# Optimization experiments

Measured on AMD Instinct MI355X. Metric: run time of the kernel, lower is better.

The kernel has to match this reference:

```python
import jax, jax.numpy as jnp
import numpy as np

B, S, D = 2, 1024, 1024
R = 512          # rank (attn) == knowledge_rank
N = 32           # neurons per pool (6 pools)
DS = 64          # router d_space
TOP_K = 4
N_HEADS = 16
LN_EPS = 1e-6


def _ln(x, scale, bias):
    mu = jnp.mean(x, axis=-1, keepdims=True)
    var = jnp.mean(jnp.square(x - mu), axis=-1, keepdims=True)
    return (x - mu) * jax.lax.rsqrt(var + LN_EPS) * scale + bias


def _topk_sparsify(w, k):
    vals, idx = jax.lax.top_k(w, k)
    oh = jax.nn.one_hot(idx, w.shape[-1], dtype=w.dtype)
    sp = (oh * vals[..., None]).sum(axis=-2)
    return sp / (sp.sum(axis=-1, keepdims=True) + 1e-8)


def _feature(x, neurons, w):
    # x:[B,S,D] neurons:[N,D,R] w:[B,S,N] -> [B,S,R]; dense [B,S,N,R] intermediate (the kernel target)
    all_h = jnp.einsum('bsd,ndr->bsnr', x, neurons)
    return jnp.einsum('bsnr,bsn->bsr', all_h, w)


def _restore(h, neurons, w):
    # h:[B,S,R] neurons:[N,R,D] w:[B,S,N] -> [B,S,D]
    all_o = jnp.einsum('bsr,nrd->bsnd', h, neurons)
    return jnp.einsum('bsnd,bsn->bsd', all_o, w)


def _route(h, emb_seg, k):
    logits = jnp.einsum('bsd,nd->bsn', h, emb_seg)
    return _topk_sparsify(jax.nn.softmax(logits, axis=-1), k)


def setup_inputs():
    key = jax.random.key(0)
    ks = jax.random.split(key, 16)
    sn = lambda k, sh: jax.random.normal(k, sh, jnp.float32) * 0.02
    return {
        'x': jax.random.normal(ks[0], (B, S, D), jnp.float32),
        'f_qk': sn(ks[1], (N, D, R)),
        'f_v': sn(ks[2], (N, D, R)),
        'r_qk': sn(ks[3], (N, R, D)),
        'r_v': sn(ks[4], (N, R, D)),
        'f_know': sn(ks[5], (N, D, R)),
        'r_know': sn(ks[6], (N, R, D)),
        'neuron_emb': sn(ks[7], (6 * N, DS)),
        'W_all': sn(ks[8], (D, 6 * DS)),
        'b_all': jnp.zeros((6 * DS,), jnp.float32),
        'W_fk': sn(ks[9], (D, DS)),
        'b_fk': jnp.zeros((DS,), jnp.float32),
        'W_rk': sn(ks[10], (D, DS)),
        'b_rk': jnp.zeros((DS,), jnp.float32),
        'W_o': sn(ks[11], (D, D)),
        'ln1_s': jnp.ones((D,), jnp.float32),
        'ln1_b': jnp.zeros((D,), jnp.float32),
        'ln2_s': jnp.ones((D,), jnp.float32),
        'ln2_b': jnp.zeros((D,), jnp.float32),
        'top_k': TOP_K,
        'n_heads': N_HEADS,
    }


def reference(x, f_qk, f_v, r_qk, r_v, f_know, r_know, neuron_emb,
              W_all, b_all, W_fk, b_fk, W_rk, b_rk, W_o,
              ln1_s, ln1_b, ln2_s, ln2_b, top_k, n_heads):
    Bx, Sx, Dm = x.shape
    n = f_qk.shape[0]
    emb = neuron_emb / (jnp.linalg.norm(neuron_emb, axis=-1, keepdims=True) + 1e-8)
    e_fqk, e_fv, e_rqk, e_rv, e_fk, e_rk = [emb[i * n:(i + 1) * n] for i in range(6)]

    # --- attention circuit (pre-norm) ---
    nx = _ln(x, ln1_s, ln1_b)
    h_all = nx @ W_all + b_all                    # [B,S,6*DS]
    h_fq, h_fk_, h_fv, h_rq, h_rk_, h_rv = jnp.split(h_all, 6, axis=-1)
    w_fq = _route(h_fq, e_fqk, top_k)             # Q/K share the qk neuron pools
    w_fk = _route(h_fk_, e_fqk, top_k)
    w_fv = _route(h_fv, e_fv, top_k)
    w_rq = _route(h_rq, e_rqk, top_k)
    w_rk = _route(h_rk_, e_rqk, top_k)
    w_rv = _route(h_rv, e_rv, top_k)

    Q = _restore(_feature(nx, f_qk, w_fq), r_qk, w_rq)
    K = _restore(_feature(nx, f_qk, w_fk), r_qk, w_rk)
    V = _restore(_feature(nx, f_v, w_fv), r_v, w_rv)

    d_head = Dm // n_heads
    Q = Q.reshape(Bx, Sx, n_heads, d_head).transpose(0, 2, 1, 3)
    K = K.reshape(Bx, Sx, n_heads, d_head).transpose(0, 2, 1, 3)
    V = V.reshape(Bx, Sx, n_heads, d_head).transpose(0, 2, 1, 3)
    scores = jnp.einsum('bhsd,bhtd->bhst', Q, K) / jnp.sqrt(jnp.float32(d_head))
    causal = jnp.tril(jnp.ones((Sx, Sx), dtype=jnp.bool_))
    scores = jnp.where(causal, scores, jnp.finfo(scores.dtype).min)
    attn = jax.nn.softmax(scores, axis=-1)
    out = jnp.einsum('bhst,bhtd->bhsd', attn, V).transpose(0, 2, 1, 3).reshape(Bx, Sx, Dm)
    x = x + out @ W_o

    # --- knowledge circuit (pre-norm) ---
    nx2 = _ln(x, ln2_s, ln2_b)
    w_fknow = _route(nx2 @ W_fk + b_fk, e_fk, top_k)
    w_rknow = _route(nx2 @ W_rk + b_rk, e_rk, top_k)
    x = x + _restore(_feature(nx2, f_know, w_fknow), r_know, w_rknow)
    return x
```

## Files before the change

kernel.cpp:

```cpp
#include <hip/hip_runtime.h>
#include <hip/hip_bf16.h>
#include <cstdint>

#define BS     2048
#define DMODEL 1024
#define RANK   512
#define NEXP   32
#define DSP    64
#define NHEAD  16
#define DHEAD  64
#define SEQ    1024
#define BATCH  2
#define HALL_N 384
#define WSTR   ((size_t)BS * NEXP)
#define LSTR   ((size_t)NEXP * BS)

typedef unsigned short u16;
typedef unsigned int u32;
typedef __attribute__((ext_vector_type(8))) short short8;
typedef __attribute__((ext_vector_type(4))) float f32x4;

__device__ __forceinline__ u16 bfbits(float x) {
  __hip_bfloat16 h = __float2bfloat16(x);
  return __builtin_bit_cast(u16, h);
}
__device__ __forceinline__ float b2f(u16 u) {
  unsigned int x = (unsigned int)u << 16;
  return __builtin_bit_cast(float, x);
}

__global__ void ln_kernel(const float* __restrict__ x,
                          const float* __restrict__ sc,
                          const float* __restrict__ bi,
                          float* __restrict__ out,
                          u16* __restrict__ outb) {
  int tok = blockIdx.x;
  int t = threadIdx.x;
  const float4* xr = reinterpret_cast<const float4*>(x + (size_t)tok * DMODEL);
  float4 v = xr[t];
  float s = v.x + v.y + v.z + v.w;
  float q = v.x * v.x + v.y * v.y + v.z * v.z + v.w * v.w;
#pragma unroll
  for (int off = 32; off > 0; off >>= 1) {
    s += __shfl_xor(s, off);
    q += __shfl_xor(q, off);
  }
  __shared__ float red[8];
  int wid = t >> 6;
  if ((t & 63) == 0) { red[wid] = s; red[4 + wid] = q; }
  __syncthreads();
  s = red[0] + red[1] + red[2] + red[3];
  q = red[4] + red[5] + red[6] + red[7];
  float mu = s * (1.f / DMODEL);
  float var = q * (1.f / DMODEL) - mu * mu;
  float inv = rsqrtf(var + 1e-6f);
  float4 scv = reinterpret_cast<const float4*>(sc)[t];
  float4 biv = reinterpret_cast<const float4*>(bi)[t];
  float4 r;
  r.x = (v.x - mu) * inv * scv.x + biv.x;
  r.y = (v.y - mu) * inv * scv.y + biv.y;
  r.z = (v.z - mu) * inv * scv.z + biv.z;
  r.w = (v.w - mu) * inv * scv.w + biv.w;
  reinterpret_cast<float4*>(out + (size_t)tok * DMODEL)[t] = r;
  ushort4 ob;
  ob.x = bfbits(r.x); ob.y = bfbits(r.y); ob.z = bfbits(r.z); ob.w = bfbits(r.w);
  reinterpret_cast<ushort4*>(outb + (size_t)tok * DMODEL)[t] = ob;
}

__global__ void embnorm_kernel(const float* __restrict__ e, float* __restrict__ o) {
  int row = blockIdx.x;
  int lane = threadIdx.x;
  float v = e[row * DSP + lane];
  float q = v * v;
#pragma unroll
  for (int off = 32; off > 0; off >>= 1) q += __shfl_xor(q, off);
  o[row * DSP + lane] = v / (sqrtf(q) + 1e-8f);
}

__global__ __launch_bounds__(256) void gemm_splitk(const float* __restrict__ A,
                                                   const float* __restrict__ Bm,
                                                   float* __restrict__ part,
                                                   int M, int N, int K, int kchunk) {
  __shared__ float As[16][65];
  __shared__ float Bs[16][64];
  int n0 = blockIdx.x * 64;
  int m0 = blockIdx.y * 64;
  int kbeg = blockIdx.z * kchunk;
  int t = threadIdx.x;
  int tx = t & 15, ty = t >> 4;
  float c[4][4] = {};
  for (int k0 = kbeg; k0 < kbeg + kchunk; k0 += 16) {
#pragma unroll
    for (int i = 0; i < 4; i++) {
      int idx = t + i * 256;
      int m = idx >> 4, kk = idx & 15;
      As[kk][m] = A[(size_t)(m0 + m) * K + k0 + kk];
    }
#pragma unroll
    for (int i = 0; i < 4; i++) {
      int idx = t + i * 256;
      int kk = idx >> 6, nn = idx & 63;
      Bs[kk][nn] = Bm[(size_t)(k0 + kk) * N + n0 + nn];
    }
    __syncthreads();
#pragma unroll
    for (int kk = 0; kk < 16; kk++) {
      float a[4], b[4];
#pragma unroll
      for (int i = 0; i < 4; i++) a[i] = As[kk][ty + i * 16];
#pragma unroll
      for (int j = 0; j < 4; j++) b[j] = Bs[kk][tx + j * 16];
#pragma unroll
      for (int i = 0; i < 4; i++)
#pragma unroll
        for (int j = 0; j < 4; j++) c[i][j] += a[i] * b[j];
    }
    __syncthreads();
  }
  float* po = part + (size_t)blockIdx.z * M * N;
#pragma unroll
  for (int i = 0; i < 4; i++)
#pragma unroll
    for (int j = 0; j < 4; j++)
      po[(size_t)(m0 + ty + i * 16) * N + n0 + tx + j * 16] = c[i][j];
}

__global__ __launch_bounds__(256) void gemm_splitk2(const float* __restrict__ A,
                                                    const float* __restrict__ B0,
                                                    const float* __restrict__ B1,
                                                    float* __restrict__ part,
                                                    int M, int N, int K, int kchunk) {
  __shared__ float As[16][65];
  __shared__ float Bs[16][64];
  int wsel = blockIdx.z >> 3, ks = blockIdx.z & 7;
  const float* Bm = wsel ? B1 : B0;
  int n0 = blockIdx.x * 64;
  int m0 = blockIdx.y * 64;
  int kbeg = ks * kchunk;
  int t = threadIdx.x;
  int tx = t & 15, ty = t >> 4;
  float c[4][4] = {};
  for (int k0 = kbeg; k0 < kbeg + kchunk; k0 += 16) {
#pragma unroll
    for (int i = 0; i < 4; i++) {
      int idx = t + i * 256;
      int m = idx >> 4, kk = idx & 15;
      As[kk][m] = A[(size_t)(m0 + m) * K + k0 + kk];
    }
#pragma unroll
    for (int i = 0; i < 4; i++) {
      int idx = t + i * 256;
      int kk = idx >> 6, nn = idx & 63;
      Bs[kk][nn] = Bm[(size_t)(k0 + kk) * N + n0 + nn];
    }
    __syncthreads();
#pragma unroll
    for (int kk = 0; kk < 16; kk++) {
      float a[4], b[4];
#pragma unroll
      for (int i = 0; i < 4; i++) a[i] = As[kk][ty + i * 16];
#pragma unroll
      for (int j = 0; j < 4; j++) b[j] = Bs[kk][tx + j * 16];
#pragma unroll
      for (int i = 0; i < 4; i++)
#pragma unroll
        for (int j = 0; j < 4; j++) c[i][j] += a[i] * b[j];
    }
    __syncthreads();
  }
  float* po = part + (size_t)blockIdx.z * M * N;
#pragma unroll
  for (int i = 0; i < 4; i++)
#pragma unroll
    for (int j = 0; j < 4; j++)
      po[(size_t)(m0 + ty + i * 16) * N + n0 + tx + j * 16] = c[i][j];
}

__global__ void reduce_bias_kernel(const float* __restrict__ part,
                                   const float* __restrict__ bias,
                                   float* __restrict__ out,
                                   int MN, int N, int KS) {
  int i = blockIdx.x * 256 + threadIdx.x;
  if (i * 4 >= MN) return;
  float4 s = reinterpret_cast<const float4*>(part)[i];
  for (int ks = 1; ks < KS; ks++) {
    float4 p = reinterpret_cast<const float4*>(part + (size_t)ks * MN)[i];
    s.x += p.x; s.y += p.y; s.z += p.z; s.w += p.w;
  }
  int col = (i * 4) % N;
  float4 b = *reinterpret_cast<const float4*>(bias + col);
  s.x += b.x; s.y += b.y; s.z += b.z; s.w += b.w;
  reinterpret_cast<float4*>(out)[i] = s;
}

__global__ void reduce_bias2_kernel(const float* __restrict__ part,
                                    const float* __restrict__ bias0,
                                    const float* __restrict__ bias1,
                                    float* __restrict__ out,
                                    int MN, int N, int KS) {
  int wsel = blockIdx.y;
  const float* p0 = part + (size_t)wsel * KS * MN;
  const float* bias = wsel ? bias1 : bias0;
  float* o = out + (size_t)wsel * MN;
  int i = blockIdx.x * 256 + threadIdx.x;
  if (i * 4 >= MN) return;
  float4 s = reinterpret_cast<const float4*>(p0)[i];
  for (int ks = 1; ks < KS; ks++) {
    float4 p = reinterpret_cast<const float4*>(p0 + (size_t)ks * MN)[i];
    s.x += p.x; s.y += p.y; s.z += p.z; s.w += p.w;
  }
  int col = (i * 4) % N;
  float4 b = *reinterpret_cast<const float4*>(bias + col);
  s.x += b.x; s.y += b.y; s.z += b.z; s.w += b.w;
  reinterpret_cast<float4*>(o)[i] = s;
}

__global__ void route_kernel(const float* __restrict__ h, size_t roff, int ldh,
                             const float* __restrict__ embn, int R0,
                             float* __restrict__ w8) {
  int tok = blockIdx.x;
  int r = blockIdx.y;
  int gr = R0 + r;
  int pool = (gr < 2) ? 0 : (gr < 3) ? 1 : (gr < 5) ? 2 : (gr < 6) ? 3 : (gr < 7) ? 4 : 5;
  const float* e = embn + (size_t)pool * NEXP * DSP;
  const float* hr = h + (size_t)r * roff;
  float* wout = w8 + (size_t)gr * WSTR;
  int lane = threadIdx.x;
  __shared__ float hs[DSP];
  __shared__ float es[NEXP * DSP];
  hs[lane] = hr[(size_t)tok * ldh + lane];
#pragma unroll
  for (int i = 0; i < NEXP * DSP / 64; i++) es[lane + i * 64] = e[lane + i * 64];
  __syncthreads();
  float logit = -1e30f;
  if (lane < NEXP) {
    float s = 0.f;
#pragma unroll
    for (int d = 0; d < DSP; d++) s += hs[d] * es[lane * DSP + d];
    logit = s;
  }
  float mx = logit;
#pragma unroll
  for (int off = 16; off > 0; off >>= 1) mx = fmaxf(mx, __shfl_xor(mx, off));
  float p = (lane < NEXP) ? __expf(logit - mx) : 0.f;
  float sum = p;
#pragma unroll
  for (int off = 16; off > 0; off >>= 1) sum += __shfl_xor(sum, off);
  p = p / sum;
  float val = p;
  float chosen = 0.f;
  float selsum = 0.f;
#pragma unroll
  for (int it = 0; it < 4; it++) {
    float v = val;
    int vi = lane;
#pragma unroll
    for (int off = 16; off > 0; off >>= 1) {
      float ov = __shfl_xor(v, off);
      int oi = __shfl_xor(vi, off);
      if (ov > v || (ov == v && oi < vi)) { v = ov; vi = oi; }
    }
    if (lane == vi) { chosen = p; val = -1.f; }
    selsum += v;
  }
  if (lane < NEXP) wout[(size_t)tok * NEXP + lane] = chosen / (selsum + 1e-8f);
}

__global__ void bucket_kernel(const float* __restrict__ w8,
                              int* __restrict__ lists,
                              int* __restrict__ slotmap,
                              int* __restrict__ counts, int R0) {
  int n = blockIdx.x;
  int gr = R0 + blockIdx.y;
  const float* w = w8 + (size_t)gr * WSTR;
  int* list = lists + (size_t)gr * LSTR;
  int* smap = slotmap + (size_t)gr * LSTR;
  int lane = threadIdx.x;
  int base = 0;
  for (int t0 = 0; t0 < BS; t0 += 64) {
    int tok = t0 + lane;
    bool act = (w[(size_t)tok * NEXP + n] != 0.f);
    unsigned long long mask = __ballot(act);
    int pos = __popcll(mask & ((1ull << lane) - 1ull));
    if (act) {
      list[n * BS + base + pos] = tok;
      smap[n * BS + tok] = base + pos;
    }
    base += __popcll(mask);
  }
  if (lane == 0) counts[gr * NEXP + n] = base;
}

__global__ void scan32_kernel(const int* __restrict__ counts, int* __restrict__ offs) {
  int r = blockIdx.x;
  int lane = threadIdx.x;
  int c = (lane < NEXP) ? counts[r * NEXP + lane] : 0;
  int s = c;
#pragma unroll
  for (int d = 1; d < NEXP; d <<= 1) {
    int o = __shfl_up(s, d);
    if (lane >= d) s += o;
  }
  if (lane < NEXP) offs[r * NEXP + lane] = s - c;
}

#define TCOL(r, c) ((c) ^ (((((r) >> 2)) & 15) << 1))
__global__ void wconv3_kernel(const float* __restrict__ F0,
                              const float* __restrict__ F1,
                              const float* __restrict__ F2,
                              u16* __restrict__ FT, int K, int NOUT) {
  int z = blockIdx.z;
  int p = z >> 5, e = z & 31;
  const float* Fe = ((p == 0) ? F0 : (p == 1) ? F1 : F2) + (size_t)e * K * NOUT;
  u16* FTe = FT + (size_t)z * K * NOUT;
  int n0 = blockIdx.x * 64, k0 = blockIdx.y * 64;
  __shared__ u16 tile[64][66];
  int t = threadIdx.x;
  int kr = t >> 4, nc = (t & 15) * 4;
#pragma unroll
  for (int pp = 0; pp < 4; pp++) {
    int kk = kr + pp * 16;
    float4 v = *reinterpret_cast<const float4*>(Fe + (size_t)(k0 + kk) * NOUT + n0 + nc);
    tile[nc + 0][TCOL(nc + 0, kk)] = bfbits(v.x);
    tile[nc + 1][TCOL(nc + 1, kk)] = bfbits(v.y);
    tile[nc + 2][TCOL(nc + 2, kk)] = bfbits(v.z);
    tile[nc + 3][TCOL(nc + 3, kk)] = bfbits(v.w);
  }
  __syncthreads();
  int nr = t >> 2, c0 = (t & 3) * 16;
  int key = (nr >> 2) & 15;
  const u32* rowp = reinterpret_cast<const u32*>(&tile[nr][0]);
  u32 u[8];
#pragma unroll
  for (int s = 0; s < 8; s++) u[s] = rowp[((c0 >> 1) + s) ^ key];
  u16* dst = FTe + (size_t)(n0 + nr) * K + k0 + c0;
  *reinterpret_cast<uint4*>(dst) = *reinterpret_cast<uint4*>(&u[0]);
  *reinterpret_cast<uint4*>(dst + 8) = *reinterpret_cast<uint4*>(&u[4]);
}

__global__ __launch_bounds__(256) void expert_gemm_mfma(
    const u16* __restrict__ Xb,
    const u16* __restrict__ FT,
    const int* __restrict__ lists,
    const int* __restrict__ counts,
    const int* __restrict__ offsb,
    u16* __restrict__ Cout,
    int R0, int s0, int s1, int s2,
    size_t xstride, int K, int NOUT) {
  int v = blockIdx.y;
  int r = v >> 5, e = v & 31;
  int gr = R0 + r;
  int cnt = counts[gr * NEXP + e];
  int m0 = blockIdx.z * 128;
  if (m0 >= cnt) return;
  int slot = (r == 0) ? s0 : (r == 1) ? s1 : s2;
  int n0 = blockIdx.x * 64;
  const int* list = lists + (size_t)gr * LSTR + (size_t)e * BS;
  __shared__ u16 Xs[128][72];
  __shared__ u16 Fs[64][72];
  __shared__ int toks[128];
  int t = threadIdx.x;
  if (t < 128) toks[t] = (m0 + t < cnt) ? list[m0 + t] : -1;
  __syncthreads();
  const u16* X = Xb + (size_t)r * xstride;
  const u16* FTe = FT + ((size_t)(slot * NEXP + e) * NOUT + n0) * K;
  int wave = t >> 6, lane = t & 63;
  int wm = wave >> 1, wn = wave & 1;
  int lr = lane & 15, kg = lane >> 4;
  f32x4 acc[4][2] = {};
  int xri = t >> 1, xc = (t & 1) * 32;
  int tokr = toks[xri];
  const u16* xrow = X + (size_t)(tokr < 0 ? 0 : tokr) * K + xc;
  int fri = t >> 2, fc = (t & 3) * 16;
  const u16* frow = FTe + (size_t)fri * K + fc;
  short8 xv0 = {}, xv1 = {}, xv2 = {}, xv3 = {}, fv0, fv1;
  if (tokr >= 0) {
    xv0 = *reinterpret_cast<const short8*>(xrow);
    xv1 = *reinterpret_cast<const short8*>(xrow + 8);
    xv2 = *reinterpret_cast<const short8*>(xrow + 16);
    xv3 = *reinterpret_cast<const short8*>(xrow + 24);
  }
  fv0 = *reinterpret_cast<const short8*>(frow);
  fv1 = *reinterpret_cast<const short8*>(frow + 8);
  for (int k0 = 0; k0 < K; k0 += 64) {
    __syncthreads();
    *reinterpret_cast<short8*>(&Xs[xri][xc]) = xv0;
    *reinterpret_cast<short8*>(&Xs[xri][xc + 8]) = xv1;
    *reinterpret_cast<short8*>(&Xs[xri][xc + 16]) = xv2;
    *reinterpret_cast<short8*>(&Xs[xri][xc + 24]) = xv3;
    *reinterpret_cast<short8*>(&Fs[fri][fc]) = fv0;
    *reinterpret_cast<short8*>(&Fs[fri][fc + 8]) = fv1;
    __syncthreads();
    int kn = k0 + 64;
    if (kn < K) {
      if (tokr >= 0) {
        xv0 = *reinterpret_cast<const short8*>(xrow + kn);
        xv1 = *reinterpret_cast<const short8*>(xrow + kn + 8);
        xv2 = *reinterpret_cast<const short8*>(xrow + kn + 16);
        xv3 = *reinterpret_cast<const short8*>(xrow + kn + 24);
      }
      fv0 = *reinterpret_cast<const short8*>(frow + kn);
      fv1 = *reinterpret_cast<const short8*>(frow + kn + 8);
    }
#pragma unroll
    for (int kk = 0; kk < 2; kk++) {
      short8 b0 = *reinterpret_cast<const short8*>(&Fs[wn * 32 + lr][kk * 32 + kg * 8]);
      short8 b1 = *reinterpret_cast<const short8*>(&Fs[wn * 32 + 16 + lr][kk * 32 + kg * 8]);
#pragma unroll
      for (int mi = 0; mi < 4; mi++) {
        short8 a = *reinterpret_cast<const short8*>(&Xs[wm * 64 + mi * 16 + lr][kk * 32 + kg * 8]);
        acc[mi][0] = __builtin_amdgcn_mfma_f32_16x16x32_bf16(a, b0, acc[mi][0], 0, 0, 0);
        acc[mi][1] = __builtin_amdgcn_mfma_f32_16x16x32_bf16(a, b1, acc[mi][1], 0, 0, 0);
      }
    }
  }
  int gbase = r * 4 * BS + offsb[gr * NEXP + e] + m0;
#pragma unroll
  for (int mi = 0; mi < 4; mi++) {
#pragma unroll
    for (int j = 0; j < 4; j++) {
      int row = wm * 64 + mi * 16 + kg * 4 + j;
      if (toks[row] < 0) continue;
      u16* crow = Cout + (size_t)(gbase + row) * NOUT + n0 + wn * 32;
#pragma unroll
      for (int ni = 0; ni < 2; ni++)
        crow[ni * 16 + lr] = bfbits(acc[mi][ni][j]);
    }
  }
}

template <int NOUT, bool FINAL>
__global__ __launch_bounds__(256) void gather_combine(
    const u16* __restrict__ C,
    const float* __restrict__ w8base,
    const int* __restrict__ slotbase,
    const int* __restrict__ offsbase,
    const float* __restrict__ resid,
    float* __restrict__ outf,
    u16* __restrict__ outbase) {
  int tok = blockIdx.x;
  int r = blockIdx.y;
  const float* wr = w8base + (size_t)r * WSTR;
  const int* smap = slotbase + (size_t)r * LSTR;
  const int* offs = offsbase + r * NEXP;
  const u16* Cr = C + (size_t)r * 4 * BS * NOUT;
  int t = threadIdx.x;
  __shared__ float lw[4];
  __shared__ int ls[4];
  __shared__ int lcnt;
  if (t < 64) {
    float wv = (t < NEXP) ? wr[(size_t)tok * NEXP + t] : 0.f;
    bool act = wv != 0.f;
    unsigned long long mask = __ballot(act);
    int pos = __popcll(mask & ((1ull << t) - 1ull));
    if (act) { ls[pos] = offs[t] + smap[t * BS + tok]; lw[pos] = wv; }
    if (t == 0) lcnt = __popcll(mask);
  }
  __syncthreads();
  if (t < NOUT / 4) {
    float4 s = {0.f, 0.f, 0.f, 0.f};
    int cnt = lcnt;
    for (int k = 0; k < cnt; k++) {
      ushort4 v = reinterpret_cast<const ushort4*>(Cr + (size_t)ls[k] * NOUT)[t];
      float wk = lw[k];
      s.x += wk * b2f(v.x); s.y += wk * b2f(v.y);
      s.z += wk * b2f(v.z); s.w += wk * b2f(v.w);
    }
    if (FINAL) {
      float4 rr = reinterpret_cast<const float4*>(resid + (size_t)tok * NOUT)[t];
      s.x += rr.x; s.y += rr.y; s.z += rr.z; s.w += rr.w;
      reinterpret_cast<float4*>(outf + (size_t)tok * NOUT)[t] = s;
    } else {
      ushort4 o;
      o.x = bfbits(s.x); o.y = bfbits(s.y); o.z = bfbits(s.z); o.w = bfbits(s.w);
      reinterpret_cast<ushort4*>(outbase + (size_t)r * BS * NOUT + (size_t)tok * NOUT)[t] = o;
    }
  }
}

template <bool RES>
__global__ __launch_bounds__(256) void dense_gemm_mfma(
    const u16* __restrict__ Ab,
    const u16* __restrict__ BT,
    const float* __restrict__ res,
    float* __restrict__ C, int M, int N, int K) {
  int n0 = blockIdx.x * 64, m0 = blockIdx.y * 64;
  __shared__ u16 Xs[64][72];
  __shared__ u16 Fs[64][72];
  int t = threadIdx.x;
  int wave = t >> 6, lane = t & 63;
  int wm = wave >> 1, wn = wave & 1;
  int lr = lane & 15, kg = lane >> 4;
  f32x4 acc[2][2] = {};
  int srow = t >> 2, sc = (t & 3) * 16;
  const u16* xrow = Ab + (size_t)(m0 + srow) * K + sc;
  const u16* frow = BT + (size_t)(n0 + srow) * K + sc;
  for (int k0 = 0; k0 < K; k0 += 64) {
    short8 xv0 = *reinterpret_cast<const short8*>(xrow + k0);
    short8 xv1 = *reinterpret_cast<const short8*>(xrow + k0 + 8);
    short8 fv0 = *reinterpret_cast<const short8*>(frow + k0);
    short8 fv1 = *reinterpret_cast<const short8*>(frow + k0 + 8);
    __syncthreads();
    *reinterpret_cast<short8*>(&Xs[srow][sc]) = xv0;
    *reinterpret_cast<short8*>(&Xs[srow][sc + 8]) = xv1;
    *reinterpret_cast<short8*>(&Fs[srow][sc]) = fv0;
    *reinterpret_cast<short8*>(&Fs[srow][sc + 8]) = fv1;
    __syncthreads();
#pragma unroll
    for (int kk = 0; kk < 2; kk++) {
      short8 a0 = *reinterpret_cast<const short8*>(&Xs[wm * 32 + lr][kk * 32 + kg * 8]);
      short8 a1 = *reinterpret_cast<const short8*>(&Xs[wm * 32 + 16 + lr][kk * 32 + kg * 8]);
      short8 b0 = *reinterpret_cast<const short8*>(&Fs[wn * 32 + lr][kk * 32 + kg * 8]);
      short8 b1 = *reinterpret_cast<const short8*>(&Fs[wn * 32 + 16 + lr][kk * 32 + kg * 8]);
      acc[0][0] = __builtin_amdgcn_mfma_f32_16x16x32_bf16(a0, b0, acc[0][0], 0, 0, 0);
      acc[0][1] = __builtin_amdgcn_mfma_f32_16x16x32_bf16(a0, b1, acc[0][1], 0, 0, 0);
      acc[1][0] = __builtin_amdgcn_mfma_f32_16x16x32_bf16(a1, b0, acc[1][0], 0, 0, 0);
      acc[1][1] = __builtin_amdgcn_mfma_f32_16x16x32_bf16(a1, b1, acc[1][1], 0, 0, 0);
    }
  }
#pragma unroll
  for (int mi = 0; mi < 2; mi++) {
#pragma unroll
    for (int j = 0; j < 4; j++) {
      int row = m0 + wm * 32 + mi * 16 + kg * 4 + j;
#pragma unroll
      for (int ni = 0; ni < 2; ni++) {
        int col = n0 + wn * 32 + ni * 16 + lr;
        float v = acc[mi][ni][j];
        if (RES) v += res[(size_t)row * N + col];
        C[(size_t)row * N + col] = v;
      }
    }
  }
}

__global__ __launch_bounds__(256) void attn_mfma(const u16* __restrict__ Qb,
                                                 const u16* __restrict__ Kb,
                                                 const u16* __restrict__ Vb,
                                                 u16* __restrict__ Ob) {
  int qt = (gridDim.x - 1 - blockIdx.x) * 64;
  int h = blockIdx.y, b = blockIdx.z;
  int t = threadIdx.x;
  int w = t >> 6, lane = t & 63;
  int lr = lane & 15, kg = lane >> 4;
  __shared__ u16 Ks[64][72];
  __shared__ u16 Vs[64][66];
  __shared__ u16 Ps[4][16][72];
  size_t base = (size_t)(b * SEQ) * DMODEL + (size_t)h * DHEAD;
  const u16* qrow = Qb + base + (size_t)(qt + w * 16 + lr) * DMODEL + kg * 8;
  short8 aq0 = *reinterpret_cast<const short8*>(qrow);
  short8 aq1 = *reinterpret_cast<const short8*>(qrow + 32);
  float m[4], l[4];
#pragma unroll
  for (int j = 0; j < 4; j++) { m[j] = -1e30f; l[j] = 0.f; }
  f32x4 acc_o[4] = {};
  for (int kt = 0; kt <= qt; kt += 64) {
    __syncthreads();
    {
      int r = t >> 2, c0 = (t & 3) * 16;
      const u16* krow = Kb + base + (size_t)(kt + r) * DMODEL + c0;
      *reinterpret_cast<short8*>(&Ks[r][c0]) = *reinterpret_cast<const short8*>(krow);
      *reinterpret_cast<short8*>(&Ks[r][c0 + 8]) = *reinterpret_cast<const short8*>(krow + 8);
      int d = lane;
      int r0v = w * 16;
      const u16* vcol = Vb + base + (size_t)(kt + r0v) * DMODEL + d;
#pragma unroll
      for (int i = 0; i < 16; i++)
        Vs[d][r0v + i] = vcol[(size_t)i * DMODEL];
    }
    __syncthreads();
    f32x4 s[4] = {};
#pragma unroll
    for (int c = 0; c < 4; c++) {
      short8 bk0 = *reinterpret_cast<const short8*>(&Ks[c * 16 + lr][kg * 8]);
      short8 bk1 = *reinterpret_cast<const short8*>(&Ks[c * 16 + lr][32 + kg * 8]);
      s[c] = __builtin_amdgcn_mfma_f32_16x16x32_bf16(aq0, bk0, s[c], 0, 0, 0);
      s[c] = __builtin_amdgcn_mfma_f32_16x16x32_bf16(aq1, bk1, s[c], 0, 0, 0);
    }
#pragma unroll
    for (int c = 0; c < 4; c++)
#pragma unroll
      for (int j = 0; j < 4; j++) s[c][j] *= 0.125f;
    if (kt == qt) {
#pragma unroll
      for (int c = 0; c < 4; c++)
#pragma unroll
        for (int j = 0; j < 4; j++)
          if (c * 16 + lr > w * 16 + kg * 4 + j) s[c][j] = -1e30f;
    }
    float mt[4];
#pragma unroll
    for (int j = 0; j < 4; j++)
      mt[j] = fmaxf(fmaxf(s[0][j], s[1][j]), fmaxf(s[2][j], s[3][j]));
#pragma unroll
    for (int off = 1; off < 16; off <<= 1)
#pragma unroll
      for (int j = 0; j < 4; j++) mt[j] = fmaxf(mt[j], __shfl_xor(mt[j], off));
    float corr[4];
#pragma unroll
    for (int j = 0; j < 4; j++) {
      float mn = fmaxf(m[j], mt[j]);
      corr[j] = __expf(m[j] - mn);
      m[j] = mn;
      l[j] *= corr[j];
    }
#pragma unroll
    for (int di = 0; di < 4; di++)
#pragma unroll
      for (int j = 0; j < 4; j++) acc_o[di][j] *= corr[j];
    float ps[4] = {0.f, 0.f, 0.f, 0.f};
#pragma unroll
    for (int c = 0; c < 4; c++)
#pragma unroll
      for (int j = 0; j < 4; j++) {
        float p = __expf(s[c][j] - m[j]);
        ps[j] += p;
        s[c][j] = p;
      }
#pragma unroll
    for (int off = 1; off < 16; off <<= 1)
#pragma unroll
      for (int j = 0; j < 4; j++) ps[j] += __shfl_xor(ps[j], off);
#pragma unroll
    for (int j = 0; j < 4; j++) l[j] += ps[j];
#pragma unroll
    for (int c = 0; c < 4; c++)
#pragma unroll
      for (int j = 0; j < 4; j++)
        Ps[w][kg * 4 + j][c * 16 + lr] = bfbits(s[c][j]);
    short8 pa0 = *reinterpret_cast<const short8*>(&Ps[w][lr][kg * 8]);
    short8 pa1 = *reinterpret_cast<const short8*>(&Ps[w][lr][32 + kg * 8]);
#pragma unroll
    for (int di = 0; di < 4; di++) {
      short8 bv0 = *reinterpret_cast<const short8*>(&Vs[di * 16 + lr][kg * 8]);
      short8 bv1 = *reinterpret_cast<const short8*>(&Vs[di * 16 + lr][32 + kg * 8]);
      acc_o[di] = __builtin_amdgcn_mfma_f32_16x16x32_bf16(pa0, bv0, acc_o[di], 0, 0, 0);
      acc_o[di] = __builtin_amdgcn_mfma_f32_16x16x32_bf16(pa1, bv1, acc_o[di], 0, 0, 0);
    }
  }
#pragma unroll
  for (int j = 0; j < 4; j++) {
    float inv = 1.f / l[j];
    size_t rowoff = base + (size_t)(qt + w * 16 + kg * 4 + j) * DMODEL;
#pragma unroll
    for (int di = 0; di < 4; di++)
      Ob[rowoff + di * 16 + lr] = bfbits(acc_o[di][j] * inv);
  }
}

extern "C" void kernel_launch(void* const* d_in, const int* in_sizes, int n_in,
                              void* d_out, int out_size, void* d_ws, size_t ws_size,
                              hipStream_t stream) {
  const float* x    = (const float*)d_in[0];
  const float* f_qk = (const float*)d_in[1];
  const float* f_v  = (const float*)d_in[2];
  const float* r_qk = (const float*)d_in[3];
  const float* r_v  = (const float*)d_in[4];
  const float* f_kn = (const float*)d_in[5];
  const float* r_kn = (const float*)d_in[6];
  const float* nemb = (const float*)d_in[7];
  const float* W_all = (const float*)d_in[8];
  const float* b_all = (const float*)d_in[9];
  const float* W_fk  = (const float*)d_in[10];
  const float* b_fk  = (const float*)d_in[11];
  const float* W_rk  = (const float*)d_in[12];
  const float* b_rk  = (const float*)d_in[13];
  const float* W_o   = (const float*)d_in[14];
  const float* ln1s  = (const float*)d_in[15];
  const float* ln1b  = (const float*)d_in[16];
  const float* ln2s  = (const float*)d_in[17];
  const float* ln2b  = (const float*)d_in[18];

  float* ws = (float*)d_ws;
  size_t off = 0;
  auto alloc = [&](size_t nf) { float* p = ws + off; off += nf; return p; };
  float* nx      = alloc((size_t)BS * DMODEL);
  float* nx2     = alloc((size_t)BS * DMODEL);
  float* embn    = alloc(6 * NEXP * DSP);
  float* h_all   = alloc((size_t)BS * HALL_N);
  float* hk2     = alloc((size_t)2 * BS * DSP);
  float* w8      = alloc((size_t)8 * BS * NEXP);
  float* x1      = alloc((size_t)BS * DMODEL);
  float* compactFf = alloc((size_t)3 * 2 * BS * RANK);
  float* compactRf = alloc((size_t)3 * 2 * BS * DMODEL);
  int* lists   = (int*)(ws + off); off += (size_t)8 * NEXP * BS;
  int* slotmap = (int*)(ws + off); off += (size_t)8 * NEXP * BS;
  int* counts  = (int*)(ws + off); off += 8 * NEXP;
  int* offsb   = (int*)(ws + off); off += 8 * NEXP;
  u16* nxb  = (u16*)(ws + off); off += (size_t)BS * DMODEL / 2;
  u16* fqb  = (u16*)(ws + off); off += (size_t)3 * BS * RANK / 2;
  u16* fnb  = (u16*)(ws + off); off += (size_t)BS * RANK / 2;
  u16* Qbb  = (u16*)(ws + off); off += (size_t)3 * BS * DMODEL / 2;
  u16* attnOb = (u16*)(ws + off); off += (size_t)BS * DMODEL / 2;
  u16* woT  = (u16*)(ws + off); off += (size_t)DMODEL * DMODEL / 2;
  u16* wbufF = (u16*)(ws + off); off += (size_t)3 * NEXP * DMODEL * RANK / 2;
  u16* wbufR = (u16*)(ws + off); off += (size_t)3 * NEXP * RANK * DMODEL / 2;
  u16* compactF = (u16*)compactFf;
  u16* compactR = (u16*)compactRf;
  u16* fkb = fqb + (size_t)BS * RANK;
  u16* fvb = fkb + (size_t)BS * RANK;
  u16* Kbb = Qbb + (size_t)BS * DMODEL;
  u16* Vbb = Kbb + (size_t)BS * DMODEL;
  float* h_fk2 = hk2;
  float* partA = compactRf;
  float* partK = compactRf;

  embnorm_kernel<<<6 * NEXP, DSP, 0, stream>>>(nemb, embn);
  wconv3_kernel<<<dim3(RANK / 64, DMODEL / 64, 3 * NEXP), 256, 0, stream>>>(
      f_qk, f_v, f_kn, wbufF, DMODEL, RANK);
  wconv3_kernel<<<dim3(DMODEL / 64, RANK / 64, 3 * NEXP), 256, 0, stream>>>(
      r_qk, r_v, r_kn, wbufR, RANK, DMODEL);
  wconv3_kernel<<<dim3(DMODEL / 64, DMODEL / 64, 1), 256, 0, stream>>>(
      W_o, nullptr, nullptr, woT, DMODEL, DMODEL);

  ln_kernel<<<BS, 256, 0, stream>>>(x, ln1s, ln1b, nx, nxb);
  gemm_splitk<<<dim3(HALL_N / 64, BS / 64, 4), 256, 0, stream>>>(
      nx, W_all, partA, BS, HALL_N, DMODEL, DMODEL / 4);
  reduce_bias_kernel<<<(BS * HALL_N / 4 + 255) / 256, 256, 0, stream>>>(
      partA, b_all, h_all, BS * HALL_N, HALL_N, 4);

  route_kernel<<<dim3(BS, 6), 64, 0, stream>>>(h_all, DSP, HALL_N, embn, 0, w8);
  bucket_kernel<<<dim3(NEXP, 6), 64, 0, stream>>>(w8, lists, slotmap, counts, 0);
  scan32_kernel<<<6, 64, 0, stream>>>(counts, offsb);

  expert_gemm_mfma<<<dim3(RANK / 64, 3 * NEXP, BS / 128), 256, 0, stream>>>(
      nxb, wbufF, lists, counts, offsb, compactF,
      0, 0, 0, 1, 0, DMODEL, RANK);
  gather_combine<RANK, false><<<dim3(BS, 3), 256, 0, stream>>>(
      compactF, w8, slotmap, offsb, nullptr, nullptr, fqb);

  expert_gemm_mfma<<<dim3(DMODEL / 64, 3 * NEXP, BS / 128), 256, 0, stream>>>(
      fqb, wbufR, lists, counts, offsb, compactR,
      3, 0, 0, 1, (size_t)BS * RANK, RANK, DMODEL);
  gather_combine<DMODEL, false><<<dim3(BS, 3), 256, 0, stream>>>(
      compactR, w8 + 3 * WSTR, slotmap + 3 * LSTR, offsb + 3 * NEXP,
      nullptr, nullptr, Qbb);

  attn_mfma<<<dim3(SEQ / 64, NHEAD, BATCH), 256, 0, stream>>>(Qbb, Kbb, Vbb, attnOb);

  dense_gemm_mfma<true><<<dim3(DMODEL / 64, BS / 64), 256, 0, stream>>>(
      attnOb, woT, x, x1, BS, DMODEL, DMODEL);

  ln_kernel<<<BS, 256, 0, stream>>>(x1, ln2s, ln2b, nx2, nxb);
  gemm_splitk2<<<dim3(1, BS / 64, 16), 256, 0, stream>>>(
      nx2, W_fk, W_rk, partK, BS, DSP, DMODEL, DMODEL / 8);
  reduce_bias2_kernel<<<dim3((BS * DSP / 4 + 255) / 256, 2), 256, 0, stream>>>(
      partK, b_fk, b_rk, h_fk2, BS * DSP, DSP, 8);
  route_kernel<<<dim3(BS, 2), 64, 0, stream>>>(h_fk2, (size_t)BS * DSP, DSP, embn, 6, w8);
  bucket_kernel<<<dim3(NEXP, 2), 64, 0, stream>>>(w8, lists, slotmap, counts, 6);
  scan32_kernel<<<2, 64, 0, stream>>>(counts + 6 * NEXP, offsb + 6 * NEXP);

  expert_gemm_mfma<<<dim3(RANK / 64, NEXP, BS / 128), 256, 0, stream>>>(
      nxb, wbufF, lists, counts, offsb, compactF,
      6, 2, 2, 2, 0, DMODEL, RANK);
  gather_combine<RANK, false><<<dim3(BS, 1), 256, 0, stream>>>(
      compactF, w8 + 6 * WSTR, slotmap + 6 * LSTR, offsb + 6 * NEXP,
      nullptr, nullptr, fnb);
  expert_gemm_mfma<<<dim3(DMODEL / 64, NEXP, BS / 128), 256, 0, stream>>>(
      fnb, wbufR, lists, counts, offsb, compactR,
      7, 2, 2, 2, 0, RANK, DMODEL);
  gather_combine<DMODEL, true><<<dim3(BS, 1), 256, 0, stream>>>(
      compactR, w8 + 7 * WSTR, slotmap + 7 * LSTR, offsb + 7 * NEXP,
      x1, (float*)d_out, nullptr);
}
```

Measured before the change: 523.7 us.

## Fuse weight conversions into concurrent routing and expert GEMM launches

Merges the first-stage split-K routing GEMM with the bf16 conversion of the feature weights and W_o into one launch. It also merges the first expert GEMM with the restore-weight conversion, so independent work shares a grid and fills idle CUs. This cuts kernel launches and lets memory-bound conversion overlap compute-bound work. In exchange, shared memory is sized by a union, which may lower occupancy for the conversion blocks, and many expert-GEMM blocks exit early.

```diff
diff --git a/kernel.cpp b/kernel.cpp
--- a/kernel.cpp
+++ b/kernel.cpp
@@ -28,6 +28,12 @@
   unsigned int x = (unsigned int)u << 16;
   return __builtin_bit_cast(float, x);
 }
+
+struct SmemGemm { u16 Xs[128][72]; u16 Fs[64][72]; int toks[128]; };
+struct SmemWc   { u16 tile[64][66]; };
+struct SmemSk   { float As[16][65]; float Bs[16][64]; };
+union SmemSmall { SmemWc w; SmemSk s; };
+union SmemBig   { SmemGemm g; SmemWc w; };
 
 __global__ void ln_kernel(const float* __restrict__ x,
                           const float* __restrict__ sc,
@@ -77,39 +83,36 @@
   o[row * DSP + lane] = v / (sqrtf(q) + 1e-8f);
 }
 
-__global__ __launch_bounds__(256) void gemm_splitk(const float* __restrict__ A,
-                                                   const float* __restrict__ Bm,
-                                                   float* __restrict__ part,
-                                                   int M, int N, int K, int kchunk) {
-  __shared__ float As[16][65];
-  __shared__ float Bs[16][64];
-  int n0 = blockIdx.x * 64;
-  int m0 = blockIdx.y * 64;
-  int kbeg = blockIdx.z * kchunk;
+__device__ __forceinline__ void dev_splitk(const float* __restrict__ A,
+                                           const float* __restrict__ Bm,
+                                           float* __restrict__ part,
+                                           int M, int N, int K, int kchunk,
+                                           int n0, int m0, int ksb, SmemSk* ss) {
   int t = threadIdx.x;
   int tx = t & 15, ty = t >> 4;
+  int kbeg = ksb * kchunk;
   float c[4][4] = {};
   for (int k0 = kbeg; k0 < kbeg + kchunk; k0 += 16) {
 #pragma unroll
     for (int i = 0; i < 4; i++) {
       int idx = t + i * 256;
       int m = idx >> 4, kk = idx & 15;
-      As[kk][m] = A[(size_t)(m0 + m) * K + k0 + kk];
+      ss->As[kk][m] = A[(size_t)(m0 + m) * K + k0 + kk];
     }
 #pragma unroll
     for (int i = 0; i < 4; i++) {
       int idx = t + i * 256;
       int kk = idx >> 6, nn = idx & 63;
-      Bs[kk][nn] = Bm[(size_t)(k0 + kk) * N + n0 + nn];
+      ss->Bs[kk][nn] = Bm[(size_t)(k0 + kk) * N + n0 + nn];
     }
     __syncthreads();
 #pragma unroll
     for (int kk = 0; kk < 16; kk++) {
       float a[4], b[4];
 #pragma unroll
-      for (int i = 0; i < 4; i++) a[i] = As[kk][ty + i * 16];
-#pragma unroll
-      for (int j = 0; j < 4; j++) b[j] = Bs[kk][tx + j * 16];
+      for (int i = 0; i < 4; i++) a[i] = ss->As[kk][ty + i * 16];
+#pragma unroll
+      for (int j = 0; j < 4; j++) b[j] = ss->Bs[kk][tx + j * 16];
 #pragma unroll
       for (int i = 0; i < 4; i++)
 #pragma unroll
@@ -117,7 +120,7 @@
     }
     __syncthreads();
   }
-  float* po = part + (size_t)blockIdx.z * M * N;
+  float* po = part + (size_t)ksb * M * N;
 #pragma unroll
   for (int i = 0; i < 4; i++)
 #pragma unroll
@@ -130,50 +133,10 @@
                                                     const float* __restrict__ B1,
                                                     float* __restrict__ part,
                                                     int M, int N, int K, int kchunk) {
-  __shared__ float As[16][65];
-  __shared__ float Bs[16][64];
+  __shared__ SmemSk ss;
   int wsel = blockIdx.z >> 3, ks = blockIdx.z & 7;
-  const float* Bm = wsel ? B1 : B0;
-  int n0 = blockIdx.x * 64;
-  int m0 = blockIdx.y * 64;
-  int kbeg = ks * kchunk;
-  int t = threadIdx.x;
-  int tx = t & 15, ty = t >> 4;
-  float c[4][4] = {};
-  for (int k0 = kbeg; k0 < kbeg + kchunk; k0 += 16) {
-#pragma unroll
-    for (int i = 0; i < 4; i++) {
-      int idx = t + i * 256;
-      int m = idx >> 4, kk = idx & 15;
-      As[kk][m] = A[(size_t)(m0 + m) * K + k0 + kk];
-    }
-#pragma unroll
-    for (int i = 0; i < 4; i++) {
-      int idx = t + i * 256;
-      int kk = idx >> 6, nn = idx & 63;
-      Bs[kk][nn] = Bm[(size_t)(k0 + kk) * N + n0 + nn];
-    }
-    __syncthreads();
-#pragma unroll
-    for (int kk = 0; kk < 16; kk++) {
-      float a[4], b[4];
-#pragma unroll
-      for (int i = 0; i < 4; i++) a[i] = As[kk][ty + i * 16];
-#pragma unroll
-      for (int j = 0; j < 4; j++) b[j] = Bs[kk][tx + j * 16];
-#pragma unroll
-      for (int i = 0; i < 4; i++)
-#pragma unroll
-        for (int j = 0; j < 4; j++) c[i][j] += a[i] * b[j];
-    }
-    __syncthreads();
-  }
-  float* po = part + (size_t)blockIdx.z * M * N;
-#pragma unroll
-  for (int i = 0; i < 4; i++)
-#pragma unroll
-    for (int j = 0; j < 4; j++)
-      po[(size_t)(m0 + ty + i * 16) * N + n0 + tx + j * 16] = c[i][j];
+  dev_splitk(A, wsel ? B1 : B0, part + (size_t)wsel * 8 * M * N,
+             M, N, K, kchunk, blockIdx.x * 64, blockIdx.y * 64, ks, &ss);
 }
 
 __global__ void reduce_bias_kernel(const float* __restrict__ part,
@@ -305,31 +268,25 @@
 }
 
 #define TCOL(r, c) ((c) ^ (((((r) >> 2)) & 15) << 1))
-__global__ void wconv3_kernel(const float* __restrict__ F0,
-                              const float* __restrict__ F1,
-                              const float* __restrict__ F2,
-                              u16* __restrict__ FT, int K, int NOUT) {
-  int z = blockIdx.z;
-  int p = z >> 5, e = z & 31;
-  const float* Fe = ((p == 0) ? F0 : (p == 1) ? F1 : F2) + (size_t)e * K * NOUT;
-  u16* FTe = FT + (size_t)z * K * NOUT;
-  int n0 = blockIdx.x * 64, k0 = blockIdx.y * 64;
-  __shared__ u16 tile[64][66];
+__device__ __forceinline__ void dev_wconv(const float* __restrict__ Fe,
+                                          u16* __restrict__ FTe,
+                                          int K, int NOUT, int n0, int k0,
+                                          SmemWc* sw) {
   int t = threadIdx.x;
   int kr = t >> 4, nc = (t & 15) * 4;
 #pragma unroll
   for (int pp = 0; pp < 4; pp++) {
     int kk = kr + pp * 16;
     float4 v = *reinterpret_cast<const float4*>(Fe + (size_t)(k0 + kk) * NOUT + n0 + nc);
-    tile[nc + 0][TCOL(nc + 0, kk)] = bfbits(v.x);
-    tile[nc + 1][TCOL(nc + 1, kk)] = bfbits(v.y);
-    tile[nc + 2][TCOL(nc + 2, kk)] = bfbits(v.z);
-    tile[nc + 3][TCOL(nc + 3, kk)] = bfbits(v.w);
+    sw->tile[nc + 0][TCOL(nc + 0, kk)] = bfbits(v.x);
+    sw->tile[nc + 1][TCOL(nc + 1, kk)] = bfbits(v.y);
+    sw->tile[nc + 2][TCOL(nc + 2, kk)] = bfbits(v.z);
+    sw->tile[nc + 3][TCOL(nc + 3, kk)] = bfbits(v.w);
   }
   __syncthreads();
   int nr = t >> 2, c0 = (t & 3) * 16;
   int key = (nr >> 2) & 15;
-  const u32* rowp = reinterpret_cast<const u32*>(&tile[nr][0]);
+  const u32* rowp = reinterpret_cast<const u32*>(&sw->tile[nr][0]);
   u32 u[8];
 #pragma unroll
   for (int s = 0; s < 8; s++) u[s] = rowp[((c0 >> 1) + s) ^ key];
@@ -338,29 +295,20 @@
   *reinterpret_cast<uint4*>(dst + 8) = *reinterpret_cast<uint4*>(&u[4]);
 }
 
-__global__ __launch_bounds__(256) void expert_gemm_mfma(
-    const u16* __restrict__ Xb,
-    const u16* __restrict__ FT,
-    const int* __restrict__ lists,
-    const int* __restrict__ counts,
-    const int* __restrict__ offsb,
-    u16* __restrict__ Cout,
-    int R0, int s0, int s1, int s2,
-    size_t xstride, int K, int NOUT) {
-  int v = blockIdx.y;
+__device__ __forceinline__ void dev_expert_gemm(
+    const u16* __restrict__ Xb, const u16* __restrict__ FT,
+    const int* __restrict__ lists, const int* __restrict__ counts,
+    const int* __restrict__ offsb, u16* __restrict__ Cout,
+    int R0, int s0, int s1, int s2, size_t xstride, int K, int NOUT,
+    int n0, int v, int m0, SmemGemm* sg) {
   int r = v >> 5, e = v & 31;
   int gr = R0 + r;
   int cnt = counts[gr * NEXP + e];
-  int m0 = blockIdx.z * 128;
   if (m0 >= cnt) return;
   int slot = (r == 0) ? s0 : (r == 1) ? s1 : s2;
-  int n0 = blockIdx.x * 64;
   const int* list = lists + (size_t)gr * LSTR + (size_t)e * BS;
-  __shared__ u16 Xs[128][72];
-  __shared__ u16 Fs[64][72];
-  __shared__ int toks[128];
   int t = threadIdx.x;
-  if (t < 128) toks[t] = (m0 + t < cnt) ? list[m0 + t] : -1;
+  if (t < 128) sg->toks[t] = (m0 + t < cnt) ? list[m0 + t] : -1;
   __syncthreads();
   const u16* X = Xb + (size_t)r * xstride;
   const u16* FTe = FT + ((size_t)(slot * NEXP + e) * NOUT + n0) * K;
@@ -369,7 +317,7 @@
   int lr = lane & 15, kg = lane >> 4;
   f32x4 acc[4][2] = {};
   int xri = t >> 1, xc = (t & 1) * 32;
-  int tokr = toks[xri];
+  int tokr = sg->toks[xri];
   const u16* xrow = X + (size_t)(tokr < 0 ? 0 : tokr) * K + xc;
   int fri = t >> 2, fc = (t & 3) * 16;
   const u16* frow = FTe + (size_t)fri * K + fc;
@@ -384,12 +332,12 @@
   fv1 = *reinterpret_cast<const short8*>(frow + 8);
   for (int k0 = 0; k0 < K; k0 += 64) {
     __syncthreads();
-    *reinterpret_cast<short8*>(&Xs[xri][xc]) = xv0;
-    *reinterpret_cast<short8*>(&Xs[xri][xc + 8]) = xv1;
-    *reinterpret_cast<short8*>(&Xs[xri][xc + 16]) = xv2;
-    *reinterpret_cast<short8*>(&Xs[xri][xc + 24]) = xv3;
-    *reinterpret_cast<short8*>(&Fs[fri][fc]) = fv0;
-    *reinterpret_cast<short8*>(&Fs[fri][fc + 8]) = fv1;
+    *reinterpret_cast<short8*>(&sg->Xs[xri][xc]) = xv0;
+    *reinterpret_cast<short8*>(&sg->Xs[xri][xc + 8]) = xv1;
+    *reinterpret_cast<short8*>(&sg->Xs[xri][xc + 16]) = xv2;
+    *reinterpret_cast<short8*>(&sg->Xs[xri][xc + 24]) = xv3;
+    *reinterpret_cast<short8*>(&sg->Fs[fri][fc]) = fv0;
+    *reinterpret_cast<short8*>(&sg->Fs[fri][fc + 8]) = fv1;
     __syncthreads();
     int kn = k0 + 64;
     if (kn < K) {
@@ -404,11 +352,11 @@
     }
 #pragma unroll
     for (int kk = 0; kk < 2; kk++) {
-      short8 b0 = *reinterpret_cast<const short8*>(&Fs[wn * 32 + lr][kk * 32 + kg * 8]);
-      short8 b1 = *reinterpret_cast<const short8*>(&Fs[wn * 32 + 16 + lr][kk * 32 + kg * 8]);
+      short8 b0 = *reinterpret_cast<const short8*>(&sg->Fs[wn * 32 + lr][kk * 32 + kg * 8]);
+      short8 b1 = *reinterpret_cast<const short8*>(&sg->Fs[wn * 32 + 16 + lr][kk * 32 + kg * 8]);
 #pragma unroll
       for (int mi = 0; mi < 4; mi++) {
-        short8 a = *reinterpret_cast<const short8*>(&Xs[wm * 64 + mi * 16 + lr][kk * 32 + kg * 8]);
+        short8 a = *reinterpret_cast<const short8*>(&sg->Xs[wm * 64 + mi * 16 + lr][kk * 32 + kg * 8]);
         acc[mi][0] = __builtin_amdgcn_mfma_f32_16x16x32_bf16(a, b0, acc[mi][0], 0, 0, 0);
         acc[mi][1] = __builtin_amdgcn_mfma_f32_16x16x32_bf16(a, b1, acc[mi][1], 0, 0, 0);
       }
@@ -420,12 +368,66 @@
 #pragma unroll
     for (int j = 0; j < 4; j++) {
       int row = wm * 64 + mi * 16 + kg * 4 + j;
-      if (toks[row] < 0) continue;
+      if (sg->toks[row] < 0) continue;
       u16* crow = Cout + (size_t)(gbase + row) * NOUT + n0 + wn * 32;
 #pragma unroll
       for (int ni = 0; ni < 2; ni++)
         crow[ni * 16 + lr] = bfbits(acc[mi][ni][j]);
     }
+  }
+}
+
+__global__ __launch_bounds__(256) void expert_gemm_mfma(
+    const u16* __restrict__ Xb, const u16* __restrict__ FT,
+    const int* __restrict__ lists, const int* __restrict__ counts,
+    const int* __restrict__ offsb, u16* __restrict__ Cout,
+    int R0, int s0, int s1, int s2, size_t xstride, int K, int NOUT) {
+  __shared__ SmemGemm sg;
+  dev_expert_gemm(Xb, FT, lists, counts, offsb, Cout, R0, s0, s1, s2,
+                  xstride, K, NOUT, blockIdx.x * 64, blockIdx.y, blockIdx.z * 128, &sg);
+}
+
+__global__ __launch_bounds__(256) void fused1_kernel(
+    const float* __restrict__ nx, const float* __restrict__ W_all,
+    float* __restrict__ part,
+    const float* __restrict__ F0, const float* __restrict__ F1,
+    const float* __restrict__ F2, u16* __restrict__ wbufF,
+    const float* __restrict__ W_o, u16* __restrict__ woT) {
+  __shared__ SmemSmall sm;
+  int bid = blockIdx.x;
+  if (bid < 768) {
+    dev_splitk(nx, W_all, part, BS, HALL_N, DMODEL, DMODEL / 4,
+               (bid % 6) * 64, ((bid / 6) % 32) * 64, bid / 192, &sm.s);
+  } else if (bid < 13056) {
+    int wbid = bid - 768;
+    int n0 = (wbid % 8) * 64, k0 = ((wbid / 8) % 16) * 64, z = wbid / 128;
+    int p = z >> 5, e = z & 31;
+    const float* Fe = ((p == 0) ? F0 : (p == 1) ? F1 : F2) + (size_t)e * DMODEL * RANK;
+    dev_wconv(Fe, wbufF + (size_t)z * DMODEL * RANK, DMODEL, RANK, n0, k0, &sm.w);
+  } else {
+    int wbid = bid - 13056;
+    dev_wconv(W_o, woT, DMODEL, DMODEL, (wbid % 16) * 64, (wbid / 16) * 64, &sm.w);
+  }
+}
+
+__global__ __launch_bounds__(256) void fused2_kernel(
+    const u16* __restrict__ nxb, const u16* __restrict__ wbufF,
+    const int* __restrict__ lists, const int* __restrict__ counts,
+    const int* __restrict__ offsb, u16* __restrict__ compactF,
+    const float* __restrict__ R0w, const float* __restrict__ R1w,
+    const float* __restrict__ R2w, u16* __restrict__ wbufR) {
+  __shared__ SmemBig sm;
+  int bid = blockIdx.x;
+  if (bid < 12288) {
+    int gx = bid % 8, gy = (bid / 8) % 96, gz = bid / 768;
+    dev_expert_gemm(nxb, wbufF, lists, counts, offsb, compactF,
+                    0, 0, 0, 1, 0, DMODEL, RANK, gx * 64, gy, gz * 128, &sm.g);
+  } else {
+    int wbid = bid - 12288;
+    int n0 = (wbid % 16) * 64, k0 = ((wbid / 16) % 8) * 64, z = wbid / 128;
+    int p = z >> 5, e = z & 31;
+    const float* Fe = ((p == 0) ? R0w : (p == 1) ? R1w : R2w) + (size_t)e * RANK * DMODEL;
+    dev_wconv(Fe, wbufR + (size_t)z * RANK * DMODEL, RANK, DMODEL, n0, k0, &sm.w);
   }
 }
 
@@ -704,18 +706,12 @@
   float* h_fk2 = hk2;
   float* partA = compactRf;
   float* partK = compactRf;
+  (void)fkb; (void)fvb; (void)Kbb; (void)Vbb;
 
   embnorm_kernel<<<6 * NEXP, DSP, 0, stream>>>(nemb, embn);
-  wconv3_kernel<<<dim3(RANK / 64, DMODEL / 64, 3 * NEXP), 256, 0, stream>>>(
-      f_qk, f_v, f_kn, wbufF, DMODEL, RANK);
-  wconv3_kernel<<<dim3(DMODEL / 64, RANK / 64, 3 * NEXP), 256, 0, stream>>>(
-      r_qk, r_v, r_kn, wbufR, RANK, DMODEL);
-  wconv3_kernel<<<dim3(DMODEL / 64, DMODEL / 64, 1), 256, 0, stream>>>(
-      W_o, nullptr, nullptr, woT, DMODEL, DMODEL);
-
   ln_kernel<<<BS, 256, 0, stream>>>(x, ln1s, ln1b, nx, nxb);
-  gemm_splitk<<<dim3(HALL_N / 64, BS / 64, 4), 256, 0, stream>>>(
-      nx, W_all, partA, BS, HALL_N, DMODEL, DMODEL / 4);
+  fused1_kernel<<<13312, 256, 0, stream>>>(nx, W_all, partA,
+                                           f_qk, f_v, f_kn, wbufF, W_o, woT);
   reduce_bias_kernel<<<(BS * HALL_N / 4 + 255) / 256, 256, 0, stream>>>(
       partA, b_all, h_all, BS * HALL_N, HALL_N, 4);
 
@@ -723,9 +719,8 @@
   bucket_kernel<<<dim3(NEXP, 6), 64, 0, stream>>>(w8, lists, slotmap, counts, 0);
   scan32_kernel<<<6, 64, 0, stream>>>(counts, offsb);
 
-  expert_gemm_mfma<<<dim3(RANK / 64, 3 * NEXP, BS / 128), 256, 0, stream>>>(
-      nxb, wbufF, lists, counts, offsb, compactF,
-      0, 0, 0, 1, 0, DMODEL, RANK);
+  fused2_kernel<<<24576, 256, 0, stream>>>(nxb, wbufF, lists, counts, offsb, compactF,
+                                           r_qk, r_v, r_kn, wbufR);
   gather_combine<RANK, false><<<dim3(BS, 3), 256, 0, stream>>>(
       compactF, w8, slotmap, offsb, nullptr, nullptr, fqb);
 
```

Result: slower. 670.7 us (+28.1%).
